# Kernel optimization log

Measured on AMD Instinct MI355X. Metric: run time of the kernel, lower is better.

Reference implementation:

```python
import jax, jax.numpy as jnp
import numpy as np

EPS = 1e-6
NH, DK, DV = 4, 32, 32

def _ln2d(x, w, b):
    # LayerNorm2d: normalize over channel dim (dim=1), biased variance
    mu = jnp.mean(x, axis=1, keepdims=True)
    var = jnp.mean((x - mu) ** 2, axis=1, keepdims=True)
    y = (x - mu) / jnp.sqrt(var + EPS)
    return w[None, :, None, None] * y + b[None, :, None, None]

def _c1x1(w, x):
    # 1x1 conv == per-pixel matmul: w [out,in], x [B,C,H,W]
    return jnp.einsum('oc,bchw->bohw', w, x)

def _shifts(x, r):
    # All (2r+1)^2 zero-padded spatial shifts, row-major (dy,dx) like nn.Unfold.
    B, C, H, W = x.shape
    xp = jnp.pad(x, ((0, 0), (0, 0), (r, r), (r, r)))
    return jnp.stack([xp[:, :, dy:dy + H, dx:dx + W]
                      for dy in range(2 * r + 1) for dx in range(2 * r + 1)], axis=0)

def _local_attn(q, k, v, kernel):
    # Correlation-pyramid local attention: per-pixel q.k over kxk window of k,
    # softmax over window (temperature sqrt(d_k)), weighted sum of v window
    # (weights shared across channels, per ChannelAttention).
    B, _, H, W = q.shape
    r = (kernel - 1) // 2
    K2 = kernel * kernel
    qh = q.reshape(B, NH, DK, H, W)
    ks = _shifts(k, r).reshape(K2, B, NH, DK, H, W)
    corr = jnp.einsum('bncyx,jbncyx->jbnyx', qh, ks)            # [K2,B,NH,H,W]
    attn = jax.nn.softmax(corr / jnp.sqrt(jnp.float32(DK)), axis=0)
    vs = _shifts(v, r).reshape(K2, B, NH, DV, H, W)
    out = jnp.einsum('jbnyx,jbncyx->bncyx', attn, vs)
    return out.reshape(B, NH * DV, H, W)

def _mha(q, k, v, kernel, wq, wk, wv, fc, lnw, lnb):
    resid = q
    heads = _local_attn(_c1x1(wq, q), _c1x1(wk, k), _c1x1(wv, v), kernel)
    out = _c1x1(fc, heads) + resid   # residual BEFORE LN (per source)
    return _ln2d(out, lnw, lnb)

def _ffn(x, w1, b1, w2, b2, lnw, lnb):
    h = jax.nn.relu(_c1x1(w1, x) + b1[None, :, None, None])
    y = _c1x1(w2, h) + b2[None, :, None, None]
    return _ln2d(y, lnw, lnb) + x    # LN BEFORE residual add (per source)

def setup_inputs():
    key = jax.random.key(0)
    ks = jax.random.split(key, 24)
    B, C, H, W = 4, 128, 96, 96
    s = (2.0 / C) ** 0.5
    f = jnp.float32
    return {
        'input1': jax.random.normal(ks[0], (B, C, H, W), f),
        'input2': jax.random.normal(ks[1], (B, C, H, W), f),
        'wq_s': jax.random.normal(ks[2], (NH * DK, C), f) * s,
        'wk_s': jax.random.normal(ks[3], (NH * DK, C), f) * s,
        'wv_s': jax.random.normal(ks[4], (NH * DV, C), f) * s,
        'fc_s': jax.random.normal(ks[5], (C, NH * DV), f) * s,
        'lnw_s': jnp.ones((C,), f),
        'lnb_s': jnp.zeros((C,), f),
        'wq_c': jax.random.normal(ks[6], (NH * DK, C), f) * s,
        'wk_c': jax.random.normal(ks[7], (NH * DK, C), f) * s,
        'wv_c': jax.random.normal(ks[8], (NH * DV, C), f) * s,
        'fc_c': jax.random.normal(ks[9], (C, NH * DV), f) * s,
        'lnw_c': jnp.ones((C,), f),
        'lnb_c': jnp.zeros((C,), f),
        'w1': jax.random.normal(ks[10], (C, C), f) * s,
        'b1': jnp.zeros((C,), f),
        'w2': jax.random.normal(ks[11], (C, C), f) * s,
        'b2': jnp.zeros((C,), f),
        'lnw_f': jnp.ones((C,), f),
        'lnb_f': jnp.zeros((C,), f),
        'kernel': 5,
        'pad': 2,
    }

def reference(input1, input2, wq_s, wk_s, wv_s, fc_s, lnw_s, lnb_s,
              wq_c, wk_c, wv_c, fc_c, lnw_c, lnb_c,
              w1, b1, w2, b2, lnw_f, lnb_f, kernel, pad):
    slf1 = _mha(input1, input1, input1, kernel, wq_s, wk_s, wv_s, fc_s, lnw_s, lnb_s)
    slf2 = _mha(input2, input2, input2, kernel, wq_s, wk_s, wv_s, fc_s, lnw_s, lnb_s)
    crs1 = _mha(slf1, slf2, slf2, kernel, wq_c, wk_c, wv_c, fc_c, lnw_c, lnb_c)
    crs2 = _mha(slf2, slf1, slf1, kernel, wq_c, wk_c, wv_c, fc_c, lnw_c, lnb_c)
    out1 = _ffn(crs1, w1, b1, w2, b2, lnw_f, lnb_f)
    out2 = _ffn(crs2, w1, b1, w2, b2, lnw_f, lnb_f)
    return (out1, out2)
```

## Files before the change

kernel.cpp:

```cpp
#include <hip/hip_runtime.h>
#include <hip/hip_bf16.h>

typedef _Float16 h16;
typedef __attribute__((ext_vector_type(8))) _Float16 f16x8v;
typedef __attribute__((ext_vector_type(2))) _Float16 h2v;
typedef __attribute__((ext_vector_type(4))) float f32x4;
#define DI __device__ __forceinline__

constexpr int CH = 128;
constexpr int HH = 96, WW = 96;
constexpr int HW = HH * WW;
constexpr int NB = 4;
constexpr int NPIX = NB * HW;
constexpr int LDT = 136;
constexpr size_t HP = (size_t)NPIX * 32;
constexpr int GH = NPIX / 64;
constexpr int TY = 4, TX = 32;
constexpr int HYH = TY + 4, HXH = TX + 4;
constexpr int LDC = 40;
constexpr int ATB = NPIX / (TY * TX) * 4;

struct __attribute__((aligned(16))) h16x8 { h16 h[8]; };
struct Set { h16 *q, *k, *v; };

DI float h2f(h16 x) { return (float)x; }
DI h16   f2h(float x) { return (h16)x; }


DI void stage_x_cl(const h16* __restrict__ src, int ldx, h16* xl, int t) {
    #pragma unroll
    for (int i = 0; i < 4; ++i) {
        int id = t + 256 * i, px = id >> 4, cc = (id & 15) * 8;
        *reinterpret_cast<f16x8v*>(&xl[px * LDT + cc]) =
            *reinterpret_cast<const f16x8v*>(&src[(size_t)px * ldx + cc]);
    }
}

DI void stage_x_pl(const float* __restrict__ src, h16* xl, int t) {
    #pragma unroll
    for (int i = 0; i < 8; ++i) {
        int id = t + 256 * i, c = id >> 4, p4 = (id & 15) * 4;
        float4 v = *reinterpret_cast<const float4*>(&src[(size_t)c * HW + p4]);
        xl[(p4 + 0) * LDT + c] = f2h(v.x);
        xl[(p4 + 1) * LDT + c] = f2h(v.y);
        xl[(p4 + 2) * LDT + c] = f2h(v.z);
        xl[(p4 + 3) * LDT + c] = f2h(v.w);
    }
}

DI void stage_x_hm(const h16* __restrict__ Tq, h16* xl, int p0, int t) {
    const int px = t >> 2, c8 = (t & 3) * 8;
    #pragma unroll
    for (int h = 0; h < 4; ++h)
        *reinterpret_cast<f16x8v*>(&xl[px * LDT + h * 32 + c8]) =
            *reinterpret_cast<const f16x8v*>(&Tq[(size_t)h * HP + (size_t)(p0 + px) * 32 + c8]);
}

DI void stage_w(const float* __restrict__ w, h16* wl, int t) {
    #pragma unroll
    for (int i = 0; i < 8; ++i) {
        int id = t + 256 * i, o = id >> 4, cc = (id & 15) * 8;
        float4 a = *reinterpret_cast<const float4*>(&w[o * CH + cc]);
        float4 b = *reinterpret_cast<const float4*>(&w[o * CH + cc + 4]);
        h16x8 tmp;
        tmp.h[0] = f2h(a.x); tmp.h[1] = f2h(a.y); tmp.h[2] = f2h(a.z); tmp.h[3] = f2h(a.w);
        tmp.h[4] = f2h(b.x); tmp.h[5] = f2h(b.y); tmp.h[6] = f2h(b.z); tmp.h[7] = f2h(b.w);
        *reinterpret_cast<f16x8v*>(&wl[o * LDT + cc]) = *reinterpret_cast<const f16x8v*>(&tmp);
    }
}

DI void gemm64(const h16* xl, const h16* wl, int w, int l, f32x4* acc) {
    const int s = l & 15, g = l >> 4;
    #pragma unroll
    for (int ks = 0; ks < 4; ++ks) {
        f16x8v a = *reinterpret_cast<const f16x8v*>(&xl[(16 * w + s) * LDT + ks * 32 + g * 8]);
        #pragma unroll
        for (int n = 0; n < 8; ++n) {
            f16x8v b = *reinterpret_cast<const f16x8v*>(&wl[(16 * n + s) * LDT + ks * 32 + g * 8]);
            acc[n] = __builtin_amdgcn_mfma_f32_16x16x32_f16(a, b, acc[n], 0, 0, 0);
        }
    }
}

DI void qkv_epi(const f32x4* acc, h16* comp, int p0, int w, int l) {
    const int s = l & 15, g = l >> 4;
    #pragma unroll
    for (int n = 0; n < 8; ++n) {
        const int o = 16 * n + s, head = o >> 5, ch = o & 31;
        h16* pl = comp + (size_t)head * HP;
        #pragma unroll
        for (int j = 0; j < 4; ++j) {
            int px = 16 * w + 4 * g + j;
            pl[(size_t)(p0 + px) * 32 + ch] = f2h(acc[n][j]);
        }
    }
}

__global__ __launch_bounds__(256, 2)
void qkv_self_b(const float* __restrict__ x0, const float* __restrict__ x1,
                const float* __restrict__ w0, const float* __restrict__ w1_,
                const float* __restrict__ w2_, Set sA, Set sB) {
    __shared__ h16 xl[64 * LDT];
    __shared__ h16 wl[CH * LDT];
    const int bid = blockIdx.x, half = bid / GH, p0 = (bid % GH) * 64;
    const float* xv = half ? x1 : x0;
    Set S = half ? sB : sA;
    const int t = threadIdx.x;
    const int b = p0 / HW, hw0 = p0 % HW;
    stage_x_pl(xv + (size_t)b * CH * HW + hw0, xl, t);
    const int w = t >> 6, l = t & 63;
    #pragma unroll
    for (int m = 0; m < 3; ++m) {
        const float* wm = (m == 0) ? w0 : ((m == 1) ? w1_ : w2_);
        h16* comp = (m == 0) ? S.q : ((m == 1) ? S.k : S.v);
        __syncthreads();
        stage_w(wm, wl, t);
        __syncthreads();
        f32x4 acc[8];
        #pragma unroll
        for (int n = 0; n < 8; ++n) acc[n] = {0.f, 0.f, 0.f, 0.f};
        gemm64(xl, wl, w, l, acc);
        qkv_epi(acc, comp, p0, w, l);
    }
}

__global__ __launch_bounds__(256, 2)
void qkv_cross_b(const h16* __restrict__ xa, const h16* __restrict__ xb,
                 const float* __restrict__ wq, const float* __restrict__ wk,
                 const float* __restrict__ wv, Set c1, Set c2) {
    __shared__ h16 xl[64 * LDT];
    __shared__ h16 wl[CH * LDT];
    const int bid = blockIdx.x, half = bid / GH, p0 = (bid % GH) * 64;
    const h16* xq  = half ? xb : xa;
    const h16* xkv = half ? xa : xb;
    Set S = half ? c2 : c1;
    const int t = threadIdx.x;
    const int w = t >> 6, l = t & 63;

    stage_x_cl(xq + (size_t)p0 * CH, CH, xl, t);
    stage_w(wq, wl, t);
    __syncthreads();
    {
        f32x4 acc[8];
        #pragma unroll
        for (int n = 0; n < 8; ++n) acc[n] = {0.f, 0.f, 0.f, 0.f};
        gemm64(xl, wl, w, l, acc);
        qkv_epi(acc, S.q, p0, w, l);
    }
    __syncthreads();
    stage_x_cl(xkv + (size_t)p0 * CH, CH, xl, t);
    stage_w(wk, wl, t);
    __syncthreads();
    {
        f32x4 acc[8];
        #pragma unroll
        for (int n = 0; n < 8; ++n) acc[n] = {0.f, 0.f, 0.f, 0.f};
        gemm64(xl, wl, w, l, acc);
        qkv_epi(acc, S.k, p0, w, l);
    }
    __syncthreads();
    stage_w(wv, wl, t);
    __syncthreads();
    {
        f32x4 acc[8];
        #pragma unroll
        for (int n = 0; n < 8; ++n) acc[n] = {0.f, 0.f, 0.f, 0.f};
        gemm64(xl, wl, w, l, acc);
        qkv_epi(acc, S.v, p0, w, l);
    }
}

__global__ __launch_bounds__(512)
void attn5b(Set s0, Set s1) {
    __shared__ h16 kv[HYH * HXH * LDC];
    const int bid = blockIdx.x, setId = bid / ATB, id = bid - setId * ATB;
    Set S = setId ? s1 : s0;
    const int n = id & 3, tile = id >> 2;
    const int img = tile / 72, rem = tile % 72, tr = rem / 3, tc = rem % 3;
    const int y0 = tr * TY, x0 = tc * TX;
    const int t = threadIdx.x;
    const int p = t >> 2, qtr = t & 3, ch8 = qtr * 8;
    const int ty = p >> 5, tx = p & 31;
    h16* Qh = S.q + (size_t)n * HP;
    const h16* Kh = S.k + (size_t)n * HP;
    const h16* Vh = S.v + (size_t)n * HP;
    const int gp = img * HW + (y0 + ty) * WW + (x0 + tx);
    h16* qp = Qh + (size_t)gp * 32 + ch8;

    f16x8v qv = *reinterpret_cast<const f16x8v*>(qp);

    #pragma unroll
    for (int i = 0; i < 3; ++i) {
        int id2 = t + 512 * i;
        if (id2 < 1152) {
            int r = id2 / 144, c = id2 - r * 144, px = c >> 2, c8 = (c & 3) * 8;
            int y = y0 + r - 2, x = x0 + px - 2;
            f16x8v v = {0, 0, 0, 0, 0, 0, 0, 0};
            if ((unsigned)y < (unsigned)HH && (unsigned)x < (unsigned)WW)
                v = *reinterpret_cast<const f16x8v*>(&Kh[((size_t)(img * HW + y * WW + x)) * 32 + c8]);
            *reinterpret_cast<f16x8v*>(&kv[(r * HXH + px) * LDC + c8]) = v;
        }
    }
    __syncthreads();

    float corr[25];
    #pragma unroll
    for (int dy = 0; dy < 5; ++dy)
        #pragma unroll
        for (int dx = 0; dx < 5; ++dx) {
            f16x8v kvv = *reinterpret_cast<const f16x8v*>(
                &kv[((ty + dy) * HXH + tx + dx) * LDC + ch8]);
            float s;
#if __has_builtin(__builtin_amdgcn_fdot2)
            s = __builtin_amdgcn_fdot2(h2v{qv[0], qv[1]}, h2v{kvv[0], kvv[1]}, 0.f, false);
            s = __builtin_amdgcn_fdot2(h2v{qv[2], qv[3]}, h2v{kvv[2], kvv[3]}, s, false);
            s = __builtin_amdgcn_fdot2(h2v{qv[4], qv[5]}, h2v{kvv[4], kvv[5]}, s, false);
            s = __builtin_amdgcn_fdot2(h2v{qv[6], qv[7]}, h2v{kvv[6], kvv[7]}, s, false);
#else
            s = 0.f;
            #pragma unroll
            for (int e = 0; e < 8; ++e) s += h2f(qv[e]) * h2f(kvv[e]);
#endif
            s += __shfl_xor(s, 1);
            s += __shfl_xor(s, 2);
            corr[dy * 5 + dx] = s;
        }

    float m = corr[0];
    #pragma unroll
    for (int j = 1; j < 25; ++j) m = fmaxf(m, corr[j]);
    const float sc = 0.17677669529663689f;
    float sum = 0.f;
    #pragma unroll
    for (int j = 0; j < 25; ++j) {
        float e = __expf((corr[j] - m) * sc);
        corr[j] = e; sum += e;
    }
    const float inv = 1.f / sum;

    __syncthreads();
    #pragma unroll
    for (int i = 0; i < 3; ++i) {
        int id2 = t + 512 * i;
        if (id2 < 1152) {
            int r = id2 / 144, c = id2 - r * 144, px = c >> 2, c8 = (c & 3) * 8;
            int y = y0 + r - 2, x = x0 + px - 2;
            f16x8v v = {0, 0, 0, 0, 0, 0, 0, 0};
            if ((unsigned)y < (unsigned)HH && (unsigned)x < (unsigned)WW)
                v = *reinterpret_cast<const f16x8v*>(&Vh[((size_t)(img * HW + y * WW + x)) * 32 + c8]);
            *reinterpret_cast<f16x8v*>(&kv[(r * HXH + px) * LDC + c8]) = v;
        }
    }
    __syncthreads();

    float o[8];
    #pragma unroll
    for (int e = 0; e < 8; ++e) o[e] = 0.f;
    #pragma unroll
    for (int dy = 0; dy < 5; ++dy)
        #pragma unroll
        for (int dx = 0; dx < 5; ++dx) {
            const float a = corr[dy * 5 + dx];
            f16x8v v = *reinterpret_cast<const f16x8v*>(
                &kv[((ty + dy) * HXH + tx + dx) * LDC + ch8]);
            #pragma unroll
            for (int e = 0; e < 8; ++e) o[e] += a * h2f(v[e]);
        }
    h16x8 st;
    #pragma unroll
    for (int e = 0; e < 8; ++e) st.h[e] = f2h(o[e] * inv);
    *reinterpret_cast<f16x8v*>(qp) = *reinterpret_cast<const f16x8v*>(&st);
}

template<bool RPLANAR>
__global__ __launch_bounds__(256, 2)
void fcln_b(const h16* __restrict__ t0, const h16* __restrict__ t1,
            const void* __restrict__ r0, const void* __restrict__ r1,
            const float* __restrict__ wfc, const float* __restrict__ gamma,
            const float* __restrict__ beta, h16* __restrict__ o0,
            h16* __restrict__ o1) {
    __shared__ h16 xl[64 * LDT];
    __shared__ h16 wl[CH * LDT];
    const int bid = blockIdx.x, half = bid / GH, p0 = (bid % GH) * 64;
    const h16* tin = half ? t1 : t0;
    const void* residv = half ? r1 : r0;
    h16* out = half ? o1 : o0;
    const int t = threadIdx.x;
    stage_x_hm(tin, xl, p0, t);
    stage_w(wfc, wl, t);
    __syncthreads();
    const int w = t >> 6, l = t & 63, s = l & 15, g = l >> 4;
    f32x4 acc[8];
    #pragma unroll
    for (int n = 0; n < 8; ++n) acc[n] = {0.f, 0.f, 0.f, 0.f};
    gemm64(xl, wl, w, l, acc);

    const int b = p0 / HW, hw0 = p0 % HW;
    float r[8][4];
    #pragma unroll
    for (int n = 0; n < 8; ++n) {
        const int o = 16 * n + s;
        #pragma unroll
        for (int j = 0; j < 4; ++j) {
            const int px = 16 * w + 4 * g + j;
            float rv;
            if (RPLANAR)
                rv = ((const float*)residv)[(size_t)b * CH * HW + (size_t)o * HW + hw0 + px];
            else
                rv = h2f(((const h16*)residv)[(size_t)(p0 + px) * CH + o]);
            r[n][j] = acc[n][j] + rv;
        }
    }
    float gm[8], bt[8];
    #pragma unroll
    for (int n = 0; n < 8; ++n) { gm[n] = gamma[16 * n + s]; bt[n] = beta[16 * n + s]; }
    #pragma unroll
    for (int j = 0; j < 4; ++j) {
        float sm = 0.f, sq = 0.f;
        #pragma unroll
        for (int n = 0; n < 8; ++n) { float v = r[n][j]; sm += v; sq += v * v; }
        sm += __shfl_xor(sm, 1); sq += __shfl_xor(sq, 1);
        sm += __shfl_xor(sm, 2); sq += __shfl_xor(sq, 2);
        sm += __shfl_xor(sm, 4); sq += __shfl_xor(sq, 4);
        sm += __shfl_xor(sm, 8); sq += __shfl_xor(sq, 8);
        const float mu = sm * (1.f / 128.f);
        const float var = sq * (1.f / 128.f) - mu * mu;
        const float rs = rsqrtf(var + 1e-6f);
        const int px = 16 * w + 4 * g + j;
        #pragma unroll
        for (int n = 0; n < 8; ++n) {
            const int o = 16 * n + s;
            out[(size_t)(p0 + px) * CH + o] = f2h(gm[n] * (r[n][j] - mu) * rs + bt[n]);
        }
    }
}

__global__ __launch_bounds__(256, 2)
void ffn_fused(const h16* __restrict__ y0, const h16* __restrict__ y1,
               const float* __restrict__ w1m, const float* __restrict__ b1v,
               const float* __restrict__ w2m, const float* __restrict__ b2v,
               const float* __restrict__ gamma, const float* __restrict__ beta,
               float* __restrict__ o0, float* __restrict__ o1) {
    __shared__ __align__(16) char smem[64 * LDT * 2 * 2 + CH * LDT * 2];
    h16*   xl = (h16*)smem;
    h16*   hl = (h16*)(smem + 64 * LDT * 2);
    h16*   wl = (h16*)(smem + 64 * LDT * 2 * 2);
    float* ll = (float*)(smem + 64 * LDT * 2 * 2);
    const int bid = blockIdx.x, half = bid / GH, p0 = (bid % GH) * 64;
    const h16* y = half ? y1 : y0;
    float* outp = half ? o1 : o0;
    const int t = threadIdx.x;
    stage_x_cl(y + (size_t)p0 * CH, CH, xl, t);
    stage_w(w1m, wl, t);
    __syncthreads();
    const int w = t >> 6, l = t & 63, s = l & 15, g = l >> 4;
    f32x4 acc[8];
    #pragma unroll
    for (int n = 0; n < 8; ++n) acc[n] = {0.f, 0.f, 0.f, 0.f};
    gemm64(xl, wl, w, l, acc);
    #pragma unroll
    for (int n = 0; n < 8; ++n) {
        const int o = 16 * n + s;
        const float bv = b1v[o];
        #pragma unroll
        for (int j = 0; j < 4; ++j) {
            const int px = 16 * w + 4 * g + j;
            hl[px * LDT + o] = f2h(fmaxf(acc[n][j] + bv, 0.f));
        }
    }
    __syncthreads();
    stage_w(w2m, wl, t);
    __syncthreads();
    f32x4 acc2[8];
    #pragma unroll
    for (int n = 0; n < 8; ++n) acc2[n] = {0.f, 0.f, 0.f, 0.f};
    gemm64(hl, wl, w, l, acc2);

    float gm[8], bt[8], r[8][4];
    #pragma unroll
    for (int n = 0; n < 8; ++n) {
        const int o = 16 * n + s;
        gm[n] = gamma[o]; bt[n] = beta[o];
        const float bv = b2v[o];
        #pragma unroll
        for (int j = 0; j < 4; ++j) r[n][j] = acc2[n][j] + bv;
    }
    float val[8][4];
    #pragma unroll
    for (int j = 0; j < 4; ++j) {
        float sm = 0.f, sq = 0.f;
        #pragma unroll
        for (int n = 0; n < 8; ++n) { float v = r[n][j]; sm += v; sq += v * v; }
        sm += __shfl_xor(sm, 1); sq += __shfl_xor(sq, 1);
        sm += __shfl_xor(sm, 2); sq += __shfl_xor(sq, 2);
        sm += __shfl_xor(sm, 4); sq += __shfl_xor(sq, 4);
        sm += __shfl_xor(sm, 8); sq += __shfl_xor(sq, 8);
        const float mu = sm * (1.f / 128.f);
        const float var = sq * (1.f / 128.f) - mu * mu;
        const float rs = rsqrtf(var + 1e-6f);
        const int px = 16 * w + 4 * g + j;
        #pragma unroll
        for (int n = 0; n < 8; ++n) {
            const int o = 16 * n + s;
            val[n][j] = gm[n] * (r[n][j] - mu) * rs + bt[n]
                      + h2f(xl[px * LDT + o]);
        }
    }
    __syncthreads();
    #pragma unroll
    for (int n = 0; n < 8; ++n) {
        const int o = 16 * n + s;
        #pragma unroll
        for (int j = 0; j < 4; ++j) ll[o * 65 + 16 * w + 4 * g + j] = val[n][j];
    }
    __syncthreads();
    const int b = p0 / HW, hw0 = p0 % HW;
    #pragma unroll
    for (int i = 0; i < 8; ++i) {
        int id = t + 256 * i, c = id >> 4, p4 = (id & 15) * 4;
        float4 v = { ll[c * 65 + p4], ll[c * 65 + p4 + 1],
                     ll[c * 65 + p4 + 2], ll[c * 65 + p4 + 3] };
        *reinterpret_cast<float4*>(&outp[(size_t)b * CH * HW + (size_t)c * HW + hw0 + p4]) = v;
    }
}

extern "C" void kernel_launch(void* const* d_in, const int* in_sizes, int n_in,
                              void* d_out, int out_size, void* d_ws, size_t ws_size,
                              hipStream_t stream) {
    (void)in_sizes; (void)n_in; (void)out_size; (void)ws_size;
    const float* in1  = (const float*)d_in[0];
    const float* in2  = (const float*)d_in[1];
    const float* wq_s = (const float*)d_in[2];
    const float* wk_s = (const float*)d_in[3];
    const float* wv_s = (const float*)d_in[4];
    const float* fc_s = (const float*)d_in[5];
    const float* lnw_s= (const float*)d_in[6];
    const float* lnb_s= (const float*)d_in[7];
    const float* wq_c = (const float*)d_in[8];
    const float* wk_c = (const float*)d_in[9];
    const float* wv_c = (const float*)d_in[10];
    const float* fc_c = (const float*)d_in[11];
    const float* lnw_c= (const float*)d_in[12];
    const float* lnb_c= (const float*)d_in[13];
    const float* w1   = (const float*)d_in[14];
    const float* b1   = (const float*)d_in[15];
    const float* w2   = (const float*)d_in[16];
    const float* b2   = (const float*)d_in[17];
    const float* lnw_f= (const float*)d_in[18];
    const float* lnb_f= (const float*)d_in[19];

    const size_t BUF  = (size_t)NPIX * CH;
    const size_t BUFB = BUF * 2;
    char* ws = (char*)d_ws;
    h16* W0 = (h16*)(ws + 0 * BUFB);
    h16* W1 = (h16*)(ws + 1 * BUFB);
    h16* W2 = (h16*)(ws + 2 * BUFB);
    h16* W3 = (h16*)(ws + 3 * BUFB);
    h16* D0 = (h16*)d_out;
    h16* D1 = (h16*)((char*)d_out + 1 * BUFB);
    h16* D2 = (h16*)((char*)d_out + 2 * BUFB);
    h16* D3 = (h16*)((char*)d_out + 3 * BUFB);
    float* out1 = (float*)d_out;
    float* out2 = (float*)d_out + BUF;

    const dim3 B(256), BA(512);

    Set SA = {W0, W1, W2};
    Set SB = {W3, D0, D1};
    h16* X1 = D2;
    h16* X2 = D3;

    qkv_self_b<<<dim3(2 * GH), B, 0, stream>>>(in1, in2, wq_s, wk_s, wv_s, SA, SB);
    attn5b<<<dim3(2 * ATB), BA, 0, stream>>>(SA, SB);
    fcln_b<true><<<dim3(2 * GH), B, 0, stream>>>(SA.q, SB.q, in1, in2,
                                                 fc_s, lnw_s, lnb_s, X1, X2);

    Set C1 = {W0, W1, W2};
    Set C2 = {W3, D0, D1};
    qkv_cross_b<<<dim3(2 * GH), B, 0, stream>>>(X1, X2, wq_c, wk_c, wv_c, C1, C2);
    attn5b<<<dim3(2 * ATB), BA, 0, stream>>>(C1, C2);
    h16* Y1 = W1;
    h16* Y2 = W2;
    fcln_b<false><<<dim3(2 * GH), B, 0, stream>>>(C1.q, C2.q, X1, X2,
                                                  fc_c, lnw_c, lnb_c, Y1, Y2);

    ffn_fused<<<dim3(2 * GH), B, 0, stream>>>(Y1, Y2, w1, b1, w2, b2,
                                              lnw_f, lnb_f, out1, out2);
}
```

Baseline: 183.6 us.

## Halve attention threads per pixel and accumulate weighted V in packed fp16

Result: faster. 162.9 us (-11.3%).

```diff
diff --git a/kernel.cpp b/kernel.cpp
--- a/kernel.cpp
+++ b/kernel.cpp
@@ -170,7 +170,7 @@
     }
 }
 
-__global__ __launch_bounds__(512)
+__global__ __launch_bounds__(256)
 void attn5b(Set s0, Set s1) {
     __shared__ h16 kv[HYH * HXH * LDC];
     const int bid = blockIdx.x, setId = bid / ATB, id = bid - setId * ATB;
@@ -179,19 +179,25 @@
     const int img = tile / 72, rem = tile % 72, tr = rem / 3, tc = rem % 3;
     const int y0 = tr * TY, x0 = tc * TX;
     const int t = threadIdx.x;
-    const int p = t >> 2, qtr = t & 3, ch8 = qtr * 8;
+    const int p = t >> 1, half = t & 1, ch16 = half * 16;
     const int ty = p >> 5, tx = p & 31;
     h16* Qh = S.q + (size_t)n * HP;
     const h16* Kh = S.k + (size_t)n * HP;
     const h16* Vh = S.v + (size_t)n * HP;
     const int gp = img * HW + (y0 + ty) * WW + (x0 + tx);
-    h16* qp = Qh + (size_t)gp * 32 + ch8;
-
-    f16x8v qv = *reinterpret_cast<const f16x8v*>(qp);
-
-    #pragma unroll
-    for (int i = 0; i < 3; ++i) {
-        int id2 = t + 512 * i;
+    h16* qp = Qh + (size_t)gp * 32 + ch16;
+
+    f16x8v q0 = *reinterpret_cast<const f16x8v*>(qp);
+    f16x8v q1 = *reinterpret_cast<const f16x8v*>(qp + 8);
+    {
+        const h16 sc = (h16)0.17677669529663689f;
+        #pragma unroll
+        for (int e = 0; e < 8; ++e) { q0[e] *= sc; q1[e] *= sc; }
+    }
+
+    #pragma unroll
+    for (int i = 0; i < 5; ++i) {
+        int id2 = t + 256 * i;
         if (id2 < 1152) {
             int r = id2 / 144, c = id2 - r * 144, px = c >> 2, c8 = (c & 3) * 8;
             int y = y0 + r - 2, x = x0 + px - 2;
@@ -208,40 +214,45 @@
     for (int dy = 0; dy < 5; ++dy)
         #pragma unroll
         for (int dx = 0; dx < 5; ++dx) {
-            f16x8v kvv = *reinterpret_cast<const f16x8v*>(
-                &kv[((ty + dy) * HXH + tx + dx) * LDC + ch8]);
+            const h16* kp = &kv[((ty + dy) * HXH + tx + dx) * LDC + ch16];
+            f16x8v k0 = *reinterpret_cast<const f16x8v*>(kp);
+            f16x8v k1 = *reinterpret_cast<const f16x8v*>(kp + 8);
             float s;
 #if __has_builtin(__builtin_amdgcn_fdot2)
-            s = __builtin_amdgcn_fdot2(h2v{qv[0], qv[1]}, h2v{kvv[0], kvv[1]}, 0.f, false);
-            s = __builtin_amdgcn_fdot2(h2v{qv[2], qv[3]}, h2v{kvv[2], kvv[3]}, s, false);
-            s = __builtin_amdgcn_fdot2(h2v{qv[4], qv[5]}, h2v{kvv[4], kvv[5]}, s, false);
-            s = __builtin_amdgcn_fdot2(h2v{qv[6], qv[7]}, h2v{kvv[6], kvv[7]}, s, false);
+            s = __builtin_amdgcn_fdot2(h2v{q0[0], q0[1]}, h2v{k0[0], k0[1]}, 0.f, false);
+            s = __builtin_amdgcn_fdot2(h2v{q0[2], q0[3]}, h2v{k0[2], k0[3]}, s, false);
+            s = __builtin_amdgcn_fdot2(h2v{q0[4], q0[5]}, h2v{k0[4], k0[5]}, s, false);
+            s = __builtin_amdgcn_fdot2(h2v{q0[6], q0[7]}, h2v{k0[6], k0[7]}, s, false);
+            s = __builtin_amdgcn_fdot2(h2v{q1[0], q1[1]}, h2v{k1[0], k1[1]}, s, false);
+            s = __builtin_amdgcn_fdot2(h2v{q1[2], q1[3]}, h2v{k1[2], k1[3]}, s, false);
+            s = __builtin_amdgcn_fdot2(h2v{q1[4], q1[5]}, h2v{k1[4], k1[5]}, s, false);
+            s = __builtin_amdgcn_fdot2(h2v{q1[6], q1[7]}, h2v{k1[6], k1[7]}, s, false);
 #else
             s = 0.f;
             #pragma unroll
-            for (int e = 0; e < 8; ++e) s += h2f(qv[e]) * h2f(kvv[e]);
+            for (int e = 0; e < 8; ++e) s += h2f(q0[e]) * h2f(k0[e]);
+            #pragma unroll
+            for (int e = 0; e < 8; ++e) s += h2f(q1[e]) * h2f(k1[e]);
 #endif
             s += __shfl_xor(s, 1);
-            s += __shfl_xor(s, 2);
             corr[dy * 5 + dx] = s;
         }
 
     float m = corr[0];
     #pragma unroll
     for (int j = 1; j < 25; ++j) m = fmaxf(m, corr[j]);
-    const float sc = 0.17677669529663689f;
     float sum = 0.f;
     #pragma unroll
     for (int j = 0; j < 25; ++j) {
-        float e = __expf((corr[j] - m) * sc);
+        float e = __expf(corr[j] - m);
         corr[j] = e; sum += e;
     }
     const float inv = 1.f / sum;
 
     __syncthreads();
     #pragma unroll
-    for (int i = 0; i < 3; ++i) {
-        int id2 = t + 512 * i;
+    for (int i = 0; i < 5; ++i) {
+        int id2 = t + 256 * i;
         if (id2 < 1152) {
             int r = id2 / 144, c = id2 - r * 144, px = c >> 2, c8 = (c & 3) * 8;
             int y = y0 + r - 2, x = x0 + px - 2;
@@ -253,23 +264,27 @@
     }
     __syncthreads();
 
-    float o[8];
-    #pragma unroll
-    for (int e = 0; e < 8; ++e) o[e] = 0.f;
+    f16x8v o0 = {0, 0, 0, 0, 0, 0, 0, 0};
+    f16x8v o1 = {0, 0, 0, 0, 0, 0, 0, 0};
     #pragma unroll
     for (int dy = 0; dy < 5; ++dy)
         #pragma unroll
         for (int dx = 0; dx < 5; ++dx) {
-            const float a = corr[dy * 5 + dx];
-            f16x8v v = *reinterpret_cast<const f16x8v*>(
-                &kv[((ty + dy) * HXH + tx + dx) * LDC + ch8]);
-            #pragma unroll
-            for (int e = 0; e < 8; ++e) o[e] += a * h2f(v[e]);
-        }
-    h16x8 st;
-    #pragma unroll
-    for (int e = 0; e < 8; ++e) st.h[e] = f2h(o[e] * inv);
-    *reinterpret_cast<f16x8v*>(qp) = *reinterpret_cast<const f16x8v*>(&st);
+            const h16 ah = f2h(corr[dy * 5 + dx]);
+            const f16x8v av = {ah, ah, ah, ah, ah, ah, ah, ah};
+            const h16* vp = &kv[((ty + dy) * HXH + tx + dx) * LDC + ch16];
+            f16x8v v0 = *reinterpret_cast<const f16x8v*>(vp);
+            f16x8v v1 = *reinterpret_cast<const f16x8v*>(vp + 8);
+            o0 += av * v0;
+            o1 += av * v1;
+        }
+    {
+        const h16 ih = f2h(inv);
+        const f16x8v iv = {ih, ih, ih, ih, ih, ih, ih, ih};
+        o0 *= iv; o1 *= iv;
+    }
+    *reinterpret_cast<f16x8v*>(qp)     = o0;
+    *reinterpret_cast<f16x8v*>(qp + 8) = o1;
 }
 
 template<bool RPLANAR>
@@ -463,7 +478,7 @@
     float* out1 = (float*)d_out;
     float* out2 = (float*)d_out + BUF;
 
-    const dim3 B(256), BA(512);
+    const dim3 B(256), BA(256);
 
     Set SA = {W0, W1, W2};
     Set SB = {W3, D0, D1};
```
